# Kernel optimization log

Hardware: AMD Instinct MI355X
Metric: run time of the kernel (lower is better)

## Reference

```python
import jax, jax.numpy as jnp
import numpy as np

B, D, H, L = 2048, 4096, 1024, 64
LAM = 1.0  # topo_lambda


def setup_inputs() -> dict:
    key = jax.random.key(0)
    ks = jax.random.split(key, 5)
    def w(k, sh):
        fan_in = sh[0]
        return (jax.random.normal(k, sh, jnp.float32) * (1.0 / fan_in) ** 0.5)
    return {
        "x": jax.random.normal(ks[0], (B, D), jnp.float32),
        "W1": w(ks[1], (D, H)), "b1": jnp.zeros((H,), jnp.float32),
        "W2": w(ks[2], (H, L)), "b2": jnp.zeros((L,), jnp.float32),
        "W3": w(ks[3], (L, H)), "b3": jnp.zeros((H,), jnp.float32),
        "W4": w(ks[4], (H, D)), "b4": jnp.zeros((D,), jnp.float32),
        "latent_norm": jnp.ones((1,), jnp.float32),
    }


def _cdist(a):
    # pairwise euclidean distances [N, N], safe sqrt (zero grad on zero diag)
    sq = jnp.sum(a * a, axis=1)
    d2 = jnp.maximum(sq[:, None] + sq[None, :] - 2.0 * (a @ a.T), 0.0)
    pos = d2 > 0
    return jnp.where(pos, jnp.sqrt(jnp.where(pos, d2, 1.0)), 0.0)


def _mst_edges(d):
    # 0-dim persistence pairs == MST edges of the dense distance matrix.
    # Vectorized Prim's algorithm: scan of N-1 steps, O(N) work per step.
    n = d.shape[0]
    in_tree = jnp.zeros((n,), bool).at[0].set(True)
    min_dist = d[0]
    parent = jnp.zeros((n,), jnp.int32)

    def step(carry, _):
        in_tree, min_dist, parent = carry
        j = jnp.argmin(jnp.where(in_tree, jnp.inf, min_dist)).astype(jnp.int32)
        i = parent[j]
        in_tree = in_tree.at[j].set(True)
        better = (d[j] < min_dist) & ~in_tree
        min_dist = jnp.where(better, d[j], min_dist)
        parent = jnp.where(better, j, parent)
        return (in_tree, min_dist, parent), jnp.stack([i, j])

    _, edges = jax.lax.scan(step, (in_tree, min_dist, parent), None, length=n - 1)
    return edges  # [n-1, 2] int32


def _topo_signature(dx, dz):
    # pairing indices computed on detached distances (as in torch .detach())
    p1 = _mst_edges(jax.lax.stop_gradient(dx))
    p2 = _mst_edges(jax.lax.stop_gradient(dz))
    sig1 = dx[p1[:, 0], p1[:, 1]]
    sig1_2 = dz[p1[:, 0], p1[:, 1]]
    sig2 = dz[p2[:, 0], p2[:, 1]]
    sig2_1 = dx[p2[:, 0], p2[:, 1]]
    # match_edges == 'symmetric'
    return jnp.sum((sig1 - sig1_2) ** 2) + jnp.sum((sig2 - sig2_1) ** 2)


def reference(x, W1, b1, W2, b2, W3, b3, W4, b4, latent_norm):
    z = jax.nn.relu(x @ W1 + b1) @ W2 + b2            # [B, L]
    x_rec = jax.nn.relu(z @ W3 + b3) @ W4 + b4        # [B, D]
    rec_loss = jnp.mean((x_rec - x) ** 2)
    x_dist = _cdist(x)
    x_dist = x_dist / jnp.max(x_dist)
    z_dist = _cdist(z) / latent_norm[0]
    topo_loss = _topo_signature(x_dist, z_dist) / x.shape[0]
    loss = rec_loss + LAM * topo_loss
    return loss
```

## Files before the change

### kernel.cpp

```cpp
#include <hip/hip_runtime.h>
#include <hip/hip_bf16.h>

#define B_N 2048
#define D_N 4096
#define H_N 1024
#define L_N 64
#define NTILE 136
#define SPLK 4

typedef __attribute__((ext_vector_type(8))) short short8;
typedef __attribute__((ext_vector_type(4))) float float4_t;

#define ASG __attribute__((address_space(1)))
#define ASL __attribute__((address_space(3)))


__device__ inline float bf2f(unsigned short u) {
  union { unsigned u; float f; } v; v.u = ((unsigned)u) << 16; return v.f;
}
__device__ inline unsigned short f2bf(float f) {
  union { float f; unsigned u; } v; v.f = f;
  unsigned r = v.u + 0x7fffu + ((v.u >> 16) & 1u);
  return (unsigned short)(r >> 16);
}

__device__ inline float block_sum256(float v) {
  const int lane = threadIdx.x & 63, wave = threadIdx.x >> 6;
#pragma unroll
  for (int off = 32; off; off >>= 1) v += __shfl_xor(v, off);
  __shared__ float red_s[4];
  if (lane == 0) red_s[wave] = v;
  __syncthreads();
  return red_s[0] + red_s[1] + red_s[2] + red_s[3];
}

__device__ inline float block_max256(float v) {
  const int lane = threadIdx.x & 63, wave = threadIdx.x >> 6;
#pragma unroll
  for (int off = 32; off; off >>= 1) v = fmaxf(v, __shfl_xor(v, off));
  __shared__ float redm_s[4];
  if (lane == 0) redm_s[wave] = v;
  __syncthreads();
  return fmaxf(fmaxf(redm_s[0], redm_s[1]), fmaxf(redm_s[2], redm_s[3]));
}

__device__ inline void tri_idx(int b, int& tm, int& tn) {
  int m = (int)((sqrtf(8.f * (float)b + 1.f) - 1.f) * 0.5f);
  while ((m + 1) * (m + 2) / 2 <= b) ++m;
  while (m * (m + 1) / 2 > b) --m;
  tm = m;
  tn = b - m * (m + 1) / 2;
}


__global__ __launch_bounds__(256) void prep_x(const float* __restrict__ x,
                                              unsigned short* __restrict__ xb,
                                              float* __restrict__ sqx) {
  const int row = blockIdx.x;
  const int t = threadIdx.x;
  const float4* xr = (const float4*)(x + (size_t)row * D_N);
  float s = 0.f;
  for (int i = t; i < D_N / 4; i += 256) {
    float4 v = xr[i];
    s += v.x * v.x + v.y * v.y + v.z * v.z + v.w * v.w;
    ushort4 o;
    o.x = f2bf(v.x); o.y = f2bf(v.y); o.z = f2bf(v.z); o.w = f2bf(v.w);
    const int p = i >> 3;
    const int k31 = (4 * i) & 31;
    *(ushort4*)(xb + ((size_t)p * B_N + row) * 32 + k31) = o;
  }
  float tot = block_sum256(s);
  if (t == 0) sqx[row] = tot;
}

__global__ __launch_bounds__(256) void transpose_cast(const float* __restrict__ in,
                                                      unsigned short* __restrict__ out,
                                                      int R, int C) {
  __shared__ float tile[32][33];
  const int c0 = blockIdx.x * 32, r0 = blockIdx.y * 32;
  const int tx = threadIdx.x, ty = threadIdx.y;
#pragma unroll
  for (int i = 0; i < 32; i += 8)
    tile[ty + i][tx] = in[(size_t)(r0 + ty + i) * C + c0 + tx];
  __syncthreads();
#pragma unroll
  for (int i = 0; i < 32; i += 8)
    out[((size_t)(r0 >> 5) * C + c0 + ty + i) * 32 + tx] = f2bf(tile[tx][ty + i]);
}

__global__ __launch_bounds__(1024) void init_bor(float* __restrict__ accum,
                                                 int* __restrict__ comp,
                                                 int* __restrict__ cnt,
                                                 int* __restrict__ done) {
  const int t = threadIdx.x;
  if (t < 2) { accum[t] = 0.f; cnt[t] = 0; done[t] = 0; }
  for (int v = t; v < 2 * B_N; v += 1024) comp[v] = v & (B_N - 1);
}


__device__ inline void gemm_mainloop(const unsigned short* __restrict__ A,
                                     const unsigned short* __restrict__ Bt,
                                     int nrA, int nrB, int Klen, int m_base, int n_base,
                                     float4_t acc[4][4]) {
  __shared__ unsigned short lA[128 * 32];
  __shared__ unsigned short lB[128 * 32];
  const int t = threadIdx.x;
  const int wave = t >> 6;
  const int lane = t & 63;
  const int lrow = lane & 15;
  const int quad = lane >> 4;
  const int wm = (wave & 1) * 64;
  const int wn = (wave >> 1) * 64;

  const int srow = lane >> 2;
  const int scol = (lane & 3) * 8;

  for (int k0 = 0; k0 < Klen; k0 += 32) {
    const size_t pA = (size_t)(k0 >> 5) * nrA;
    const size_t pB = (size_t)(k0 >> 5) * nrB;
    __syncthreads();
#pragma unroll
    for (int q = 0; q < 2; ++q) {
      const int rbase = wave * 32 + q * 16;
      const int row = rbase + srow;
      __builtin_amdgcn_global_load_lds(
          (ASG void*)(A + (pA + m_base + row) * 32 + scol),
          (ASL void*)(lA + rbase * 32), 16, 0, 0);
      __builtin_amdgcn_global_load_lds(
          (ASG void*)(Bt + (pB + n_base + row) * 32 + scol),
          (ASL void*)(lB + rbase * 32), 16, 0, 0);
    }
    __syncthreads();
    short8 af[4], bfr[4];
#pragma unroll
    for (int f = 0; f < 4; ++f) {
      af[f]  = *(const short8*)(lA + (wm + f * 16 + lrow) * 32 + quad * 8);
      bfr[f] = *(const short8*)(lB + (wn + f * 16 + lrow) * 32 + quad * 8);
    }
#pragma unroll
    for (int fm = 0; fm < 4; ++fm)
#pragma unroll
      for (int fn = 0; fn < 4; ++fn)
        acc[fm][fn] = __builtin_amdgcn_mfma_f32_16x16x32_bf16(af[fm], bfr[fn],
                                                              acc[fm][fn], 0, 0, 0);
  }
}

__global__ __launch_bounds__(256) void gemm_splitk(const unsigned short* __restrict__ A,
                                                   const unsigned short* __restrict__ Bt,
                                                   int nrA, int nrB, int Kchunk, int N,
                                                   float* __restrict__ partial) {
  float4_t acc[4][4];
  float4_t z4 = {0.f, 0.f, 0.f, 0.f};
#pragma unroll
  for (int a = 0; a < 4; ++a)
#pragma unroll
    for (int b = 0; b < 4; ++b) acc[a][b] = z4;
  const int s = blockIdx.z;
  const int m_base = blockIdx.y * 128, n_base = blockIdx.x * 128;
  const size_t po = (size_t)(s * (Kchunk >> 5));
  gemm_mainloop(A + po * nrA * 32, Bt + po * nrB * 32, nrA, nrB, Kchunk,
                m_base, n_base, acc);
  const size_t MN = (size_t)gridDim.y * 128 * N;
  float* __restrict__ P = partial + (size_t)s * MN;
  const int t = threadIdx.x, wave = t >> 6, lane = t & 63;
  const int lrow = lane & 15, quad = lane >> 4;
  const int wm = (wave & 1) * 64, wn = (wave >> 1) * 64;
#pragma unroll
  for (int fm = 0; fm < 4; ++fm)
#pragma unroll
    for (int fn = 0; fn < 4; ++fn) {
      const int r0 = m_base + wm + fm * 16 + quad * 4;
      const int c = n_base + wn + fn * 16 + lrow;
#pragma unroll
      for (int r = 0; r < 4; ++r)
        P[(size_t)(r0 + r) * N + c] = acc[fm][fn][r];
    }
}

__global__ __launch_bounds__(256) void gemm_d2_tri(const unsigned short* __restrict__ xb,
                                                   float* __restrict__ partial) {
  float4_t acc[4][4];
  float4_t z4 = {0.f, 0.f, 0.f, 0.f};
#pragma unroll
  for (int a = 0; a < 4; ++a)
#pragma unroll
    for (int b = 0; b < 4; ++b) acc[a][b] = z4;
  const int s = blockIdx.z;
  int tm, tn;
  tri_idx(blockIdx.x, tm, tn);
  const size_t po = (size_t)(s * ((D_N / SPLK) >> 5)) * B_N * 32;
  gemm_mainloop(xb + po, xb + po, B_N, B_N, D_N / SPLK, tm * 128, tn * 128, acc);
  float* __restrict__ P = partial + ((size_t)s * NTILE + blockIdx.x) * 16384;
  const int t = threadIdx.x, wave = t >> 6, lane = t & 63;
  const int lrow = lane & 15, quad = lane >> 4;
  const int wm = (wave & 1) * 64, wn = (wave >> 1) * 64;
#pragma unroll
  for (int fm = 0; fm < 4; ++fm)
#pragma unroll
    for (int fn = 0; fn < 4; ++fn) {
      const int lr0 = wm + fm * 16 + quad * 4;
      const int lc = wn + fn * 16 + lrow;
#pragma unroll
      for (int r = 0; r < 4; ++r)
        P[(lr0 + r) * 128 + lc] = acc[fm][fn][r];
    }
}

__global__ __launch_bounds__(256) void fin_bias_relu(const float* __restrict__ partial,
                                                     const float* __restrict__ bias,
                                                     unsigned short* __restrict__ out) {
  const size_t MN = (size_t)B_N * H_N;
  const size_t i4 = ((size_t)blockIdx.x * 256 + threadIdx.x) * 4;
  float4 a = *(const float4*)(partial + i4);
#pragma unroll
  for (int s = 1; s < SPLK; ++s) {
    float4 p = *(const float4*)(partial + s * MN + i4);
    a.x += p.x; a.y += p.y; a.z += p.z; a.w += p.w;
  }
  const int row = (int)(i4 >> 10);
  const int k = (int)(i4 & (H_N - 1));
  float4 b = *(const float4*)(bias + k);
  ushort4 o;
  o.x = f2bf(fmaxf(a.x + b.x, 0.f));
  o.y = f2bf(fmaxf(a.y + b.y, 0.f));
  o.z = f2bf(fmaxf(a.z + b.z, 0.f));
  o.w = f2bf(fmaxf(a.w + b.w, 0.f));
  *(ushort4*)(out + ((size_t)(k >> 5) * B_N + row) * 32 + (k & 31)) = o;
}

__global__ __launch_bounds__(256) void fin_d2_tri(const float* __restrict__ partial,
                                                  const float* __restrict__ sq,
                                                  float* __restrict__ Out,
                                                  unsigned* __restrict__ max_slot) {
  const int tile = blockIdx.y;
  const int c0 = blockIdx.x * 32;
  int tm, tn;
  tri_idx(tile, tm, tn);
  __shared__ float lds[32][132];
  const int t = threadIdx.x;
  const int cc = (t & 7) * 4;
  float lmax = 0.f;
#pragma unroll
  for (int q = 0; q < 4; ++q) {
    const int r = (t >> 3) + 32 * q;
    const float* base = partial + (size_t)tile * 16384 + r * 128 + c0 + cc;
    float4 a = *(const float4*)base;
#pragma unroll
    for (int s = 1; s < SPLK; ++s) {
      float4 p = *(const float4*)(base + (size_t)s * NTILE * 16384);
      a.x += p.x; a.y += p.y; a.z += p.z; a.w += p.w;
    }
    const int i = tm * 128 + r;
    const float si = sq[i];
    float4 sj = *(const float4*)(sq + tn * 128 + c0 + cc);
    float4 v;
    v.x = fmaxf(si + sj.x - 2.f * a.x, 0.f);
    v.y = fmaxf(si + sj.y - 2.f * a.y, 0.f);
    v.z = fmaxf(si + sj.z - 2.f * a.z, 0.f);
    v.w = fmaxf(si + sj.w - 2.f * a.w, 0.f);
    *(float4*)(Out + (size_t)i * B_N + tn * 128 + c0 + cc) = v;
    lds[cc + 0][r] = v.x;
    lds[cc + 1][r] = v.y;
    lds[cc + 2][r] = v.z;
    lds[cc + 3][r] = v.w;
    lmax = fmaxf(lmax, fmaxf(fmaxf(v.x, v.y), fmaxf(v.z, v.w)));
  }
  __syncthreads();
#pragma unroll
  for (int m = 0; m < 4; ++m) {
    const int lin = t + 256 * m;
    const int cc2 = lin >> 5;
    const int r4 = (lin & 31) * 4;
    float4 w = *(const float4*)(&lds[cc2][r4]);
    *(float4*)(Out + (size_t)(tn * 128 + c0 + cc2) * B_N + tm * 128 + r4) = w;
  }
  float tot = block_max256(lmax);
  if (t == 0) atomicMax(max_slot, __float_as_uint(tot));
}

__global__ __launch_bounds__(256) void gemm_recloss(const unsigned short* __restrict__ A,
                                                    const unsigned short* __restrict__ Bt,
                                                    const float* __restrict__ bias,
                                                    const float* __restrict__ Xref,
                                                    float* __restrict__ acc_slot) {
  float4_t acc[4][4];
  float4_t z4 = {0.f, 0.f, 0.f, 0.f};
#pragma unroll
  for (int a = 0; a < 4; ++a)
#pragma unroll
    for (int b = 0; b < 4; ++b) acc[a][b] = z4;
  const int m_base = blockIdx.y * 128, n_base = blockIdx.x * 128;
  gemm_mainloop(A, Bt, B_N, D_N, H_N, m_base, n_base, acc);
  const int t = threadIdx.x, wave = t >> 6, lane = t & 63;
  const int lrow = lane & 15, quad = lane >> 4;
  const int wm = (wave & 1) * 64, wn = (wave >> 1) * 64;
  float local = 0.f;
#pragma unroll
  for (int fm = 0; fm < 4; ++fm)
#pragma unroll
    for (int fn = 0; fn < 4; ++fn) {
      const int r0 = m_base + wm + fm * 16 + quad * 4;
      const int c = n_base + wn + fn * 16 + lrow;
      const float bc = bias[c];
#pragma unroll
      for (int r = 0; r < 4; ++r) {
        float v = acc[fm][fn][r] + bc - Xref[(size_t)(r0 + r) * D_N + c];
        local += v * v;
      }
    }
  float tot = block_sum256(local);
  if (t == 0) atomicAdd(acc_slot, tot);
}


__global__ __launch_bounds__(256) void g2_k(const unsigned short* __restrict__ h1b,
                                            const float* __restrict__ W2,
                                            const float* __restrict__ b2,
                                            float* __restrict__ z,
                                            float* __restrict__ sqz) {
  const int col = threadIdx.x & 63;
  const int row = blockIdx.x * 4 + (threadIdx.x >> 6);
  float a0 = 0.f, a1 = 0.f, a2 = 0.f, a3 = 0.f;
  for (int p = 0; p < H_N / 32; ++p) {
    const unsigned short* hb = h1b + ((size_t)p * B_N + row) * 32;
    const float* wb = W2 + (p * 32) * L_N + col;
#pragma unroll
    for (int k2 = 0; k2 < 32; k2 += 4) {
      a0 += bf2f(hb[k2 + 0]) * wb[(k2 + 0) * L_N];
      a1 += bf2f(hb[k2 + 1]) * wb[(k2 + 1) * L_N];
      a2 += bf2f(hb[k2 + 2]) * wb[(k2 + 2) * L_N];
      a3 += bf2f(hb[k2 + 3]) * wb[(k2 + 3) * L_N];
    }
  }
  const float zv = (a0 + a1) + (a2 + a3) + b2[col];
  z[(size_t)row * L_N + col] = zv;
  float s = zv * zv;
#pragma unroll
  for (int off = 32; off; off >>= 1) s += __shfl_xor(s, off);
  if (col == 0) sqz[row] = s;
}

__global__ __launch_bounds__(256) void g3_k(const float* __restrict__ z,
                                            const float* __restrict__ W3,
                                            const float* __restrict__ b3,
                                            unsigned short* __restrict__ h2b) {
  const int t = threadIdx.x;
  const int col = blockIdx.y * 256 + t;
  const int r0 = blockIdx.x * 4;
  __shared__ float zr[4][64];
  zr[t >> 6][t & 63] = z[(size_t)(r0 + (t >> 6)) * L_N + (t & 63)];
  __syncthreads();
  const float bc = b3[col];
  float a0 = bc, a1 = bc, a2 = bc, a3 = bc;
#pragma unroll 8
  for (int k = 0; k < 64; ++k) {
    float w = W3[k * H_N + col];
    a0 += zr[0][k] * w;
    a1 += zr[1][k] * w;
    a2 += zr[2][k] * w;
    a3 += zr[3][k] * w;
  }
  const size_t base = ((size_t)(col >> 5) * B_N) * 32 + (col & 31);
  h2b[base + (size_t)(r0 + 0) * 32] = f2bf(fmaxf(a0, 0.f));
  h2b[base + (size_t)(r0 + 1) * 32] = f2bf(fmaxf(a1, 0.f));
  h2b[base + (size_t)(r0 + 2) * 32] = f2bf(fmaxf(a2, 0.f));
  h2b[base + (size_t)(r0 + 3) * 32] = f2bf(fmaxf(a3, 0.f));
}

__global__ __launch_bounds__(256) void d2z_k(const float* __restrict__ z,
                                             const float* __restrict__ sqz,
                                             float* __restrict__ d2z) {
  const int bi = blockIdx.y * 16, bj = blockIdx.x * 16;
  __shared__ float zi[16][65], zj[16][65];
  const int t = threadIdx.x;
  for (int idx = t; idx < 16 * 64; idx += 256) {
    const int r = idx >> 6, c = idx & 63;
    zi[r][c] = z[(size_t)(bi + r) * L_N + c];
    zj[r][c] = z[(size_t)(bj + r) * L_N + c];
  }
  __syncthreads();
  const int ti = t >> 4, tj = t & 15;
  float dot = 0.f;
#pragma unroll 8
  for (int k = 0; k < 64; ++k) dot += zi[ti][k] * zj[tj][k];
  float v = fmaxf(sqz[bi + ti] + sqz[bj + tj] - 2.f * dot, 0.f);
  d2z[(size_t)(bi + ti) * B_N + bj + tj] = v;
}

__global__ __launch_bounds__(256) void bor_scan(const float* __restrict__ d2x,
                                                const float* __restrict__ d2z,
                                                const int* __restrict__ comp,
                                                unsigned long long* __restrict__ rowbest,
                                                const int* __restrict__ done) {
  const int tree = blockIdx.y;
  if (done[tree]) return;
  const float* __restrict__ d2 = tree ? d2z : d2x;
  const int* __restrict__ cp = comp + tree * B_N;
  const int i = blockIdx.x;
  const int t = threadIdx.x;
  const int ci = cp[i];
  const float* __restrict__ row = d2 + (size_t)i * B_N;
  const unsigned ibase = (unsigned)(i << 11);
  unsigned long long k = ~0ull;
#pragma unroll
  for (int m = 0; m < 2; ++m) {
    const int j4 = (t + m * 256) * 4;
    float4 dv = *(const float4*)(row + j4);
    int4 cj = *(const int4*)(cp + j4);
    if (cj.x != ci) {
      unsigned long long key = (((unsigned long long)__float_as_uint(dv.x)) << 32) | (ibase | (unsigned)(j4 + 0));
      k = key < k ? key : k;
    }
    if (cj.y != ci) {
      unsigned long long key = (((unsigned long long)__float_as_uint(dv.y)) << 32) | (ibase | (unsigned)(j4 + 1));
      k = key < k ? key : k;
    }
    if (cj.z != ci) {
      unsigned long long key = (((unsigned long long)__float_as_uint(dv.z)) << 32) | (ibase | (unsigned)(j4 + 2));
      k = key < k ? key : k;
    }
    if (cj.w != ci) {
      unsigned long long key = (((unsigned long long)__float_as_uint(dv.w)) << 32) | (ibase | (unsigned)(j4 + 3));
      k = key < k ? key : k;
    }
  }
  const int lane = t & 63, wave = t >> 6;
#pragma unroll
  for (int off = 32; off; off >>= 1) {
    unsigned long long o = __shfl_xor(k, off);
    k = o < k ? o : k;
  }
  __shared__ unsigned long long wmin[4];
  if (lane == 0) wmin[wave] = k;
  __syncthreads();
  if (t == 0) {
    unsigned long long a = wmin[0] < wmin[1] ? wmin[0] : wmin[1];
    unsigned long long b = wmin[2] < wmin[3] ? wmin[2] : wmin[3];
    rowbest[tree * B_N + i] = (a < b) ? a : b;
  }
}

__global__ __launch_bounds__(1024) void bor_merge(const unsigned long long* __restrict__ rowbest,
                                                  int* __restrict__ comp,
                                                  int2* __restrict__ edges,
                                                  int* __restrict__ cnt,
                                                  int* __restrict__ done) {
  const int tree = blockIdx.x;
  if (done[tree]) return;
  const unsigned long long* __restrict__ rb = rowbest + tree * B_N;
  int* __restrict__ cp = comp + tree * B_N;
  int2* __restrict__ eo = edges + (size_t)tree * (B_N - 1);
  int* __restrict__ cn = cnt + tree;
  __shared__ unsigned long long bc[B_N];
  __shared__ int hk[B_N];
  __shared__ int allsame;
  const int t = threadIdx.x;

#pragma unroll
  for (int q = 0; q < 2; ++q) bc[t + q * 1024] = ~0ull;
  __syncthreads();

#pragma unroll
  for (int q = 0; q < 2; ++q) {
    const int i = t + q * 1024;
    const unsigned long long key = rb[i];
    if (key != ~0ull) atomicMin(&bc[cp[i]], key);
  }
  __syncthreads();

  unsigned long long mykey[2];
#pragma unroll
  for (int q = 0; q < 2; ++q) {
    const int c = t + q * 1024;
    const unsigned long long key = bc[c];
    mykey[q] = key;
    int h = c;
    if (key != ~0ull) h = cp[(unsigned)key & (unsigned)(B_N - 1)];
    hk[c] = h;
  }
  __syncthreads();

  int rloc[2];
#pragma unroll
  for (int q = 0; q < 2; ++q) {
    const int c = t + q * 1024;
    const unsigned long long key = mykey[q];
    const int h = hk[c];
    const int hh = hk[h];
    const bool valid = key != ~0ull;
    const bool two = (h != c) && (hh == c);
    rloc[q] = (two && c < h) ? c : h;
    if (valid && (!two || c < h)) {
      int e = atomicAdd(cn, 1);
      eo[e] = make_int2((int)((key >> 11) & (unsigned)(B_N - 1)),
                        (int)(key & (unsigned)(B_N - 1)));
    }
  }
  __syncthreads();
#pragma unroll
  for (int q = 0; q < 2; ++q) hk[t + q * 1024] = rloc[q];
  if (t == 0) allsame = 1;
  __syncthreads();

  for (int it = 0; it < 11; ++it) {
    const int v0 = hk[hk[t]];
    const int v1 = hk[hk[t + 1024]];
    __syncthreads();
    hk[t] = v0;
    hk[t + 1024] = v1;
    __syncthreads();
  }

#pragma unroll
  for (int q = 0; q < 2; ++q) {
    const int v = t + q * 1024;
    cp[v] = hk[cp[v]];
  }
  __syncthreads();
  const int c0v = cp[0];
  if (cp[t] != c0v || cp[t + 1024] != c0v) allsame = 0;
  __syncthreads();
  if (t == 0 && allsame) done[tree] = 1;
}

__global__ __launch_bounds__(256) void final_k(const float* __restrict__ d2x,
                                               const float* __restrict__ d2z,
                                               const int2* __restrict__ edges,
                                               const float* __restrict__ accum,
                                               const float* __restrict__ latent_norm,
                                               float* __restrict__ out) {
  const int t = threadIdx.x;
  const float maxd = sqrtf(__uint_as_float(((const unsigned*)accum)[1]));
  const float inv_maxd = 1.0f / maxd;
  const float inv_ln = 1.0f / latent_norm[0];
  float local = 0.f;
  for (int e = t; e < 2 * (B_N - 1); e += 256) {
    int2 ij = edges[e];
    size_t idx = (size_t)ij.x * B_N + ij.y;
    float xd = sqrtf(d2x[idx]) * inv_maxd;
    float zd = sqrtf(d2z[idx]) * inv_ln;
    float d = xd - zd;
    local += d * d;
  }
  float topo = block_sum256(local);
  if (t == 0)
    out[0] = accum[0] * (1.0f / ((float)B_N * (float)D_N)) + topo * (1.0f / (float)B_N);
}

extern "C" void kernel_launch(void* const* d_in, const int* in_sizes, int n_in,
                              void* d_out, int out_size, void* d_ws, size_t ws_size,
                              hipStream_t stream) {
  const float* x  = (const float*)d_in[0];
  const float* W1 = (const float*)d_in[1];
  const float* b1 = (const float*)d_in[2];
  const float* W2 = (const float*)d_in[3];
  const float* b2 = (const float*)d_in[4];
  const float* W3 = (const float*)d_in[5];
  const float* b3 = (const float*)d_in[6];
  const float* W4 = (const float*)d_in[7];
  const float* b4 = (const float*)d_in[8];
  const float* latent_norm = (const float*)d_in[9];
  float* out = (float*)d_out;

  char* ws = (char*)d_ws;
  size_t off = 0;
  auto alloc = [&](size_t bytes) {
    size_t o = off;
    off += (bytes + 255) & ~(size_t)255;
    return o;
  };
  unsigned short* xb   = (unsigned short*)(ws + alloc((size_t)B_N * D_N * 2));
  unsigned short* w1bt = (unsigned short*)(ws + alloc((size_t)H_N * D_N * 2));
  unsigned short* w4bt = (unsigned short*)(ws + alloc((size_t)D_N * H_N * 2));
  unsigned short* h1b  = (unsigned short*)(ws + alloc((size_t)B_N * H_N * 2));
  unsigned short* h2b  = (unsigned short*)(ws + alloc((size_t)B_N * H_N * 2));
  float* z    = (float*)(ws + alloc((size_t)B_N * L_N * 4));
  float* sqx  = (float*)(ws + alloc((size_t)B_N * 4));
  float* sqz  = (float*)(ws + alloc((size_t)B_N * 4));
  float* d2x  = (float*)(ws + alloc((size_t)B_N * B_N * 4));
  float* d2z  = (float*)(ws + alloc((size_t)B_N * B_N * 4));
  int2* edges = (int2*)(ws + alloc((size_t)2 * (B_N - 1) * sizeof(int2)));
  float* accum = (float*)(ws + alloc(256));
  int* comp   = (int*)(ws + alloc((size_t)2 * B_N * 4));
  unsigned long long* rowbest = (unsigned long long*)(ws + alloc((size_t)2 * B_N * 8));
  int* cnt    = (int*)(ws + alloc(256));
  int* done   = (int*)(ws + alloc(256));
  float* parts = (float*)(ws + alloc((size_t)SPLK * NTILE * 16384 * 4));

  init_bor<<<1, 1024, 0, stream>>>(accum, comp, cnt, done);
  prep_x<<<B_N, 256, 0, stream>>>(x, xb, sqx);
  transpose_cast<<<dim3(H_N / 32, D_N / 32), dim3(32, 8), 0, stream>>>(W1, w1bt, D_N, H_N);
  transpose_cast<<<dim3(D_N / 32, H_N / 32), dim3(32, 8), 0, stream>>>(W4, w4bt, H_N, D_N);

  gemm_splitk<<<dim3(H_N / 128, B_N / 128, SPLK), 256, 0, stream>>>(
      xb, w1bt, B_N, H_N, D_N / SPLK, H_N, parts);
  fin_bias_relu<<<(B_N * H_N) / 1024, 256, 0, stream>>>(parts, b1, h1b);

  g2_k<<<B_N / 4, 256, 0, stream>>>(h1b, W2, b2, z, sqz);
  g3_k<<<dim3(B_N / 4, H_N / 256), 256, 0, stream>>>(z, W3, b3, h2b);
  gemm_recloss<<<dim3(D_N / 128, B_N / 128), 256, 0, stream>>>(h2b, w4bt, b4, x, accum);

  gemm_d2_tri<<<dim3(NTILE, 1, SPLK), 256, 0, stream>>>(xb, parts);
  fin_d2_tri<<<dim3(4, NTILE), 256, 0, stream>>>(parts, sqx, d2x, (unsigned*)(accum + 1));

  d2z_k<<<dim3(B_N / 16, B_N / 16), 256, 0, stream>>>(z, sqz, d2z);

  for (int r = 0; r < 11; ++r) {
    bor_scan<<<dim3(B_N, 2), 256, 0, stream>>>(d2x, d2z, comp, rowbest, done);
    bor_merge<<<2, 1024, 0, stream>>>(rowbest, comp, edges, cnt, done);
  }
  final_k<<<1, 256, 0, stream>>>(d2x, d2z, edges, accum, latent_norm, out);
}
```

Measured before the change: 427.2 us.

## Precompute per-row nearest-neighbor lists to shortcut Boruvka row scans; merge setup kernels

Adds a top-16 nearest-neighbor kernel per row for both distance matrices. Each Boruvka scan round first checks these cached neighbors and skips the full 2048-wide row read when one lies in a different component. The init, prep and two transpose kernels are also merged into fewer launches. The cost is one extra full pass over both distance matrices plus 16 serial block reductions per row, paid back only if later rounds mostly take the fast path.

```diff
diff --git a/kernel.cpp b/kernel.cpp
--- a/kernel.cpp
+++ b/kernel.cpp
@@ -7,13 +7,13 @@
 #define L_N 64
 #define NTILE 136
 #define SPLK 4
+#define NNK 16
 
 typedef __attribute__((ext_vector_type(8))) short short8;
 typedef __attribute__((ext_vector_type(4))) float float4_t;
 
 #define ASG __attribute__((address_space(1)))
 #define ASL __attribute__((address_space(3)))
-
 
 __device__ inline float bf2f(unsigned short u) {
   union { unsigned u; float f; } v; v.u = ((unsigned)u) << 16; return v.f;
@@ -55,9 +55,18 @@
 
 __global__ __launch_bounds__(256) void prep_x(const float* __restrict__ x,
                                               unsigned short* __restrict__ xb,
-                                              float* __restrict__ sqx) {
+                                              float* __restrict__ sqx,
+                                              float* __restrict__ accum,
+                                              int* __restrict__ comp,
+                                              int* __restrict__ cnt,
+                                              int* __restrict__ done) {
   const int row = blockIdx.x;
   const int t = threadIdx.x;
+  if (row == B_N) {
+    if (t < 2) { accum[t] = 0.f; cnt[t] = 0; done[t] = 0; }
+    for (int v = t; v < 2 * B_N; v += 256) comp[v] = v & (B_N - 1);
+    return;
+  }
   const float4* xr = (const float4*)(x + (size_t)row * D_N);
   float s = 0.f;
   for (int i = t; i < D_N / 4; i += 256) {
@@ -73,11 +82,18 @@
   if (t == 0) sqx[row] = tot;
 }
 
-__global__ __launch_bounds__(256) void transpose_cast(const float* __restrict__ in,
-                                                      unsigned short* __restrict__ out,
-                                                      int R, int C) {
+__global__ __launch_bounds__(256) void transpose2(const float* __restrict__ W1,
+                                                  const float* __restrict__ W4,
+                                                  unsigned short* __restrict__ w1bt,
+                                                  unsigned short* __restrict__ w4bt) {
   __shared__ float tile[32][33];
-  const int c0 = blockIdx.x * 32, r0 = blockIdx.y * 32;
+  int b = blockIdx.x;
+  const float* in;
+  unsigned short* out;
+  int C, bx, by;
+  if (b < 4096) { in = W1; out = w1bt; C = H_N; bx = b & 31;  by = b >> 5; }
+  else { b -= 4096; in = W4; out = w4bt; C = D_N; bx = b & 127; by = b >> 7; }
+  const int c0 = bx * 32, r0 = by * 32;
   const int tx = threadIdx.x, ty = threadIdx.y;
 #pragma unroll
   for (int i = 0; i < 32; i += 8)
@@ -86,15 +102,6 @@
 #pragma unroll
   for (int i = 0; i < 32; i += 8)
     out[((size_t)(r0 >> 5) * C + c0 + ty + i) * 32 + tx] = f2bf(tile[tx][ty + i]);
-}
-
-__global__ __launch_bounds__(1024) void init_bor(float* __restrict__ accum,
-                                                 int* __restrict__ comp,
-                                                 int* __restrict__ cnt,
-                                                 int* __restrict__ done) {
-  const int t = threadIdx.x;
-  if (t < 2) { accum[t] = 0.f; cnt[t] = 0; done[t] = 0; }
-  for (int v = t; v < 2 * B_N; v += 1024) comp[v] = v & (B_N - 1);
 }
 
 
@@ -388,9 +395,55 @@
   d2z[(size_t)(bi + ti) * B_N + bj + tj] = v;
 }
 
+__global__ __launch_bounds__(256) void topk_k(const float* __restrict__ d2x,
+                                              const float* __restrict__ d2z,
+                                              unsigned long long* __restrict__ nn) {
+  const int tree = blockIdx.y;
+  const float* __restrict__ d2 = tree ? d2z : d2x;
+  const int i = blockIdx.x;
+  const int t = threadIdx.x;
+  const float* __restrict__ row = d2 + (size_t)i * B_N;
+  const unsigned ibase = (unsigned)(i << 11);
+  float4 v0 = *(const float4*)(row + t * 8);
+  float4 v1 = *(const float4*)(row + t * 8 + 4);
+  unsigned long long key[8];
+  const float vv[8] = {v0.x, v0.y, v0.z, v0.w, v1.x, v1.y, v1.z, v1.w};
+#pragma unroll
+  for (int q = 0; q < 8; ++q) {
+    const int j = t * 8 + q;
+    key[q] = (j == i) ? ~0ull
+                      : ((((unsigned long long)__float_as_uint(vv[q])) << 32) |
+                         (ibase | (unsigned)j));
+  }
+  unsigned long long* __restrict__ out = nn + ((size_t)tree * B_N + i) * NNK;
+  __shared__ unsigned long long wmin_s[4];
+  const int lane = t & 63, wave = t >> 6;
+  for (int p = 0; p < NNK; ++p) {
+    unsigned long long k = key[0];
+#pragma unroll
+    for (int q = 1; q < 8; ++q) k = key[q] < k ? key[q] : k;
+#pragma unroll
+    for (int off = 32; off; off >>= 1) {
+      unsigned long long o = __shfl_xor(k, off);
+      k = o < k ? o : k;
+    }
+    if (lane == 0) wmin_s[wave] = k;
+    __syncthreads();
+    unsigned long long a = wmin_s[0] < wmin_s[1] ? wmin_s[0] : wmin_s[1];
+    unsigned long long b = wmin_s[2] < wmin_s[3] ? wmin_s[2] : wmin_s[3];
+    const unsigned long long w = a < b ? a : b;
+    if (t == 0) out[p] = w;
+#pragma unroll
+    for (int q = 0; q < 8; ++q)
+      if (key[q] == w) key[q] = ~0ull;
+    __syncthreads();
+  }
+}
+
 __global__ __launch_bounds__(256) void bor_scan(const float* __restrict__ d2x,
                                                 const float* __restrict__ d2z,
                                                 const int* __restrict__ comp,
+                                                const unsigned long long* __restrict__ nn,
                                                 unsigned long long* __restrict__ rowbest,
                                                 const int* __restrict__ done) {
   const int tree = blockIdx.y;
@@ -400,6 +453,27 @@
   const int i = blockIdx.x;
   const int t = threadIdx.x;
   const int ci = cp[i];
+  __shared__ unsigned long long fastkey;
+  __shared__ int needfull;
+  if (t < 64) {
+    unsigned long long k = ~0ull;
+    bool cross = false;
+    if (t < NNK) {
+      k = nn[((size_t)tree * B_N + i) * NNK + t];
+      cross = cp[(unsigned)k & (unsigned)(B_N - 1)] != ci;
+    }
+    const unsigned long long m = __ballot(cross);
+    if (t == 0) needfull = (m == 0ull);
+    if (m) {
+      const int wl = __builtin_ctzll(m);
+      if (t == wl) fastkey = k;
+    }
+  }
+  __syncthreads();
+  if (!needfull) {
+    if (t == 0) rowbest[tree * B_N + i] = fastkey;
+    return;
+  }
   const float* __restrict__ row = d2 + (size_t)i * B_N;
   const unsigned ibase = (unsigned)(i << 11);
   unsigned long long k = ~0ull;
@@ -584,14 +658,13 @@
   float* accum = (float*)(ws + alloc(256));
   int* comp   = (int*)(ws + alloc((size_t)2 * B_N * 4));
   unsigned long long* rowbest = (unsigned long long*)(ws + alloc((size_t)2 * B_N * 8));
+  unsigned long long* nn = (unsigned long long*)(ws + alloc((size_t)2 * B_N * NNK * 8));
   int* cnt    = (int*)(ws + alloc(256));
   int* done   = (int*)(ws + alloc(256));
   float* parts = (float*)(ws + alloc((size_t)SPLK * NTILE * 16384 * 4));
 
-  init_bor<<<1, 1024, 0, stream>>>(accum, comp, cnt, done);
-  prep_x<<<B_N, 256, 0, stream>>>(x, xb, sqx);
-  transpose_cast<<<dim3(H_N / 32, D_N / 32), dim3(32, 8), 0, stream>>>(W1, w1bt, D_N, H_N);
-  transpose_cast<<<dim3(D_N / 32, H_N / 32), dim3(32, 8), 0, stream>>>(W4, w4bt, H_N, D_N);
+  prep_x<<<B_N + 1, 256, 0, stream>>>(x, xb, sqx, accum, comp, cnt, done);
+  transpose2<<<8192, dim3(32, 8), 0, stream>>>(W1, W4, w1bt, w4bt);
 
   gemm_splitk<<<dim3(H_N / 128, B_N / 128, SPLK), 256, 0, stream>>>(
       xb, w1bt, B_N, H_N, D_N / SPLK, H_N, parts);
@@ -606,8 +679,9 @@
 
   d2z_k<<<dim3(B_N / 16, B_N / 16), 256, 0, stream>>>(z, sqz, d2z);
 
+  topk_k<<<dim3(B_N, 2), 256, 0, stream>>>(d2x, d2z, nn);
   for (int r = 0; r < 11; ++r) {
-    bor_scan<<<dim3(B_N, 2), 256, 0, stream>>>(d2x, d2z, comp, rowbest, done);
+    bor_scan<<<dim3(B_N, 2), 256, 0, stream>>>(d2x, d2z, comp, nn, rowbest, done);
     bor_merge<<<2, 1024, 0, stream>>>(rowbest, comp, edges, cnt, done);
   }
   final_k<<<1, 256, 0, stream>>>(d2x, d2z, edges, accum, latent_norm, out);
```

Result: slower. 462.0 us (+8.1%).

## Merge independent kernels into combined launches and skip unchanged Boruvka row scans

Applied to the files above, without the earlier changes.

Independent kernels are merged into shared launches that dispatch on block index: the prep/cast/init kernels, the two split-K GEMMs, the two finalize kernels, g3 with d2z, and the recon-loss GEMM with the first Boruvka scan. This cuts launch count and lets independent work fill the GPU together. The G1 and D2 GEMMs now use separate partial buffers so they can run in the same launch. bor_scan also skips a row when its previous best edge still points to another component, since that row's minimum cannot have changed. This skip depends on rowbest staying valid across rounds, and merging a GEMM with the row scan can leave some blocks imbalanced.

```diff
diff --git a/kernel.cpp b/kernel.cpp
--- a/kernel.cpp
+++ b/kernel.cpp
@@ -14,7 +14,6 @@
 #define ASG __attribute__((address_space(1)))
 #define ASL __attribute__((address_space(3)))
 
-
 __device__ inline float bf2f(unsigned short u) {
   union { unsigned u; float f; } v; v.u = ((unsigned)u) << 16; return v.f;
 }
@@ -52,33 +51,53 @@
   tn = b - m * (m + 1) / 2;
 }
 
-
-__global__ __launch_bounds__(256) void prep_x(const float* __restrict__ x,
-                                              unsigned short* __restrict__ xb,
-                                              float* __restrict__ sqx) {
-  const int row = blockIdx.x;
-  const int t = threadIdx.x;
-  const float4* xr = (const float4*)(x + (size_t)row * D_N);
-  float s = 0.f;
-  for (int i = t; i < D_N / 4; i += 256) {
-    float4 v = xr[i];
-    s += v.x * v.x + v.y * v.y + v.z * v.z + v.w * v.w;
-    ushort4 o;
-    o.x = f2bf(v.x); o.y = f2bf(v.y); o.z = f2bf(v.z); o.w = f2bf(v.w);
-    const int p = i >> 3;
-    const int k31 = (4 * i) & 31;
-    *(ushort4*)(xb + ((size_t)p * B_N + row) * 32 + k31) = o;
-  }
-  float tot = block_sum256(s);
-  if (t == 0) sqx[row] = tot;
-}
-
-__global__ __launch_bounds__(256) void transpose_cast(const float* __restrict__ in,
-                                                      unsigned short* __restrict__ out,
-                                                      int R, int C) {
+__global__ __launch_bounds__(256) void mega_prep(const float* __restrict__ x,
+                                                 const float* __restrict__ W1,
+                                                 const float* __restrict__ W4,
+                                                 unsigned short* __restrict__ xb,
+                                                 unsigned short* __restrict__ w1bt,
+                                                 unsigned short* __restrict__ w4bt,
+                                                 float* __restrict__ sqx,
+                                                 float* __restrict__ accum,
+                                                 int* __restrict__ comp,
+                                                 unsigned long long* __restrict__ rowbest,
+                                                 int* __restrict__ cnt,
+                                                 int* __restrict__ done) {
+  const int b = blockIdx.x;
+  const int t = threadIdx.x;
+  if (b < B_N) {
+    const float4* xr = (const float4*)(x + (size_t)b * D_N);
+    float s = 0.f;
+    for (int i = t; i < D_N / 4; i += 256) {
+      float4 v = xr[i];
+      s += v.x * v.x + v.y * v.y + v.z * v.z + v.w * v.w;
+      ushort4 o;
+      o.x = f2bf(v.x); o.y = f2bf(v.y); o.z = f2bf(v.z); o.w = f2bf(v.w);
+      const int p = i >> 3;
+      const int k31 = (4 * i) & 31;
+      *(ushort4*)(xb + ((size_t)p * B_N + b) * 32 + k31) = o;
+    }
+    float tot = block_sum256(s);
+    if (t == 0) sqx[b] = tot;
+    return;
+  }
+  if (b == B_N) {
+    if (t < 2) { accum[t] = 0.f; cnt[t] = 0; done[t] = 0; }
+    for (int v = t; v < 2 * B_N; v += 256) {
+      comp[v] = v & (B_N - 1);
+      rowbest[v] = ~0ull;
+    }
+    return;
+  }
+  int tb = b - (B_N + 1);
+  const float* in;
+  unsigned short* out;
+  int C, bx, by;
+  if (tb < 4096) { in = W1; out = w1bt; C = H_N; bx = tb & 31;  by = tb >> 5; }
+  else { tb -= 4096; in = W4; out = w4bt; C = D_N; bx = tb & 127; by = tb >> 7; }
+  const int c0 = bx * 32, r0 = by * 32;
+  const int tx = t & 31, ty = t >> 5;
   __shared__ float tile[32][33];
-  const int c0 = blockIdx.x * 32, r0 = blockIdx.y * 32;
-  const int tx = threadIdx.x, ty = threadIdx.y;
 #pragma unroll
   for (int i = 0; i < 32; i += 8)
     tile[ty + i][tx] = in[(size_t)(r0 + ty + i) * C + c0 + tx];
@@ -87,16 +106,6 @@
   for (int i = 0; i < 32; i += 8)
     out[((size_t)(r0 >> 5) * C + c0 + ty + i) * 32 + tx] = f2bf(tile[tx][ty + i]);
 }
-
-__global__ __launch_bounds__(1024) void init_bor(float* __restrict__ accum,
-                                                 int* __restrict__ comp,
-                                                 int* __restrict__ cnt,
-                                                 int* __restrict__ done) {
-  const int t = threadIdx.x;
-  if (t < 2) { accum[t] = 0.f; cnt[t] = 0; done[t] = 0; }
-  for (int v = t; v < 2 * B_N; v += 1024) comp[v] = v & (B_N - 1);
-}
-
 
 __device__ inline void gemm_mainloop(const unsigned short* __restrict__ A,
                                      const unsigned short* __restrict__ Bt,
@@ -111,7 +120,6 @@
   const int quad = lane >> 4;
   const int wm = (wave & 1) * 64;
   const int wn = (wave >> 1) * 64;
-
   const int srow = lane >> 2;
   const int scol = (lane & 3) * 8;
 
@@ -146,105 +154,103 @@
   }
 }
 
-__global__ __launch_bounds__(256) void gemm_splitk(const unsigned short* __restrict__ A,
-                                                   const unsigned short* __restrict__ Bt,
-                                                   int nrA, int nrB, int Kchunk, int N,
-                                                   float* __restrict__ partial) {
+__global__ __launch_bounds__(256) void mega_gemm(const unsigned short* __restrict__ xb,
+                                                 const unsigned short* __restrict__ w1bt,
+                                                 float* __restrict__ partsG1,
+                                                 float* __restrict__ partsD2) {
   float4_t acc[4][4];
   float4_t z4 = {0.f, 0.f, 0.f, 0.f};
 #pragma unroll
   for (int a = 0; a < 4; ++a)
 #pragma unroll
-    for (int b = 0; b < 4; ++b) acc[a][b] = z4;
-  const int s = blockIdx.z;
-  const int m_base = blockIdx.y * 128, n_base = blockIdx.x * 128;
-  const size_t po = (size_t)(s * (Kchunk >> 5));
-  gemm_mainloop(A + po * nrA * 32, Bt + po * nrB * 32, nrA, nrB, Kchunk,
-                m_base, n_base, acc);
-  const size_t MN = (size_t)gridDim.y * 128 * N;
-  float* __restrict__ P = partial + (size_t)s * MN;
+    for (int b2 = 0; b2 < 4; ++b2) acc[a][b2] = z4;
+  const int b = blockIdx.x;
   const int t = threadIdx.x, wave = t >> 6, lane = t & 63;
   const int lrow = lane & 15, quad = lane >> 4;
   const int wm = (wave & 1) * 64, wn = (wave >> 1) * 64;
-#pragma unroll
-  for (int fm = 0; fm < 4; ++fm)
-#pragma unroll
-    for (int fn = 0; fn < 4; ++fn) {
-      const int r0 = m_base + wm + fm * 16 + quad * 4;
-      const int c = n_base + wn + fn * 16 + lrow;
-#pragma unroll
-      for (int r = 0; r < 4; ++r)
-        P[(size_t)(r0 + r) * N + c] = acc[fm][fn][r];
-    }
-}
-
-__global__ __launch_bounds__(256) void gemm_d2_tri(const unsigned short* __restrict__ xb,
-                                                   float* __restrict__ partial) {
-  float4_t acc[4][4];
-  float4_t z4 = {0.f, 0.f, 0.f, 0.f};
-#pragma unroll
-  for (int a = 0; a < 4; ++a)
-#pragma unroll
-    for (int b = 0; b < 4; ++b) acc[a][b] = z4;
-  const int s = blockIdx.z;
-  int tm, tn;
-  tri_idx(blockIdx.x, tm, tn);
-  const size_t po = (size_t)(s * ((D_N / SPLK) >> 5)) * B_N * 32;
-  gemm_mainloop(xb + po, xb + po, B_N, B_N, D_N / SPLK, tm * 128, tn * 128, acc);
-  float* __restrict__ P = partial + ((size_t)s * NTILE + blockIdx.x) * 16384;
-  const int t = threadIdx.x, wave = t >> 6, lane = t & 63;
-  const int lrow = lane & 15, quad = lane >> 4;
-  const int wm = (wave & 1) * 64, wn = (wave >> 1) * 64;
-#pragma unroll
-  for (int fm = 0; fm < 4; ++fm)
-#pragma unroll
-    for (int fn = 0; fn < 4; ++fn) {
-      const int lr0 = wm + fm * 16 + quad * 4;
-      const int lc = wn + fn * 16 + lrow;
-#pragma unroll
-      for (int r = 0; r < 4; ++r)
-        P[(lr0 + r) * 128 + lc] = acc[fm][fn][r];
-    }
-}
-
-__global__ __launch_bounds__(256) void fin_bias_relu(const float* __restrict__ partial,
-                                                     const float* __restrict__ bias,
-                                                     unsigned short* __restrict__ out) {
-  const size_t MN = (size_t)B_N * H_N;
-  const size_t i4 = ((size_t)blockIdx.x * 256 + threadIdx.x) * 4;
-  float4 a = *(const float4*)(partial + i4);
-#pragma unroll
-  for (int s = 1; s < SPLK; ++s) {
-    float4 p = *(const float4*)(partial + s * MN + i4);
-    a.x += p.x; a.y += p.y; a.z += p.z; a.w += p.w;
-  }
-  const int row = (int)(i4 >> 10);
-  const int k = (int)(i4 & (H_N - 1));
-  float4 b = *(const float4*)(bias + k);
-  ushort4 o;
-  o.x = f2bf(fmaxf(a.x + b.x, 0.f));
-  o.y = f2bf(fmaxf(a.y + b.y, 0.f));
-  o.z = f2bf(fmaxf(a.z + b.z, 0.f));
-  o.w = f2bf(fmaxf(a.w + b.w, 0.f));
-  *(ushort4*)(out + ((size_t)(k >> 5) * B_N + row) * 32 + (k & 31)) = o;
-}
-
-__global__ __launch_bounds__(256) void fin_d2_tri(const float* __restrict__ partial,
-                                                  const float* __restrict__ sq,
-                                                  float* __restrict__ Out,
-                                                  unsigned* __restrict__ max_slot) {
-  const int tile = blockIdx.y;
-  const int c0 = blockIdx.x * 32;
+
+  if (b < 512) {
+    const int s = b >> 7;
+    const int tt = b & 127;
+    const int m_base = (tt >> 3) * 128, n_base = (tt & 7) * 128;
+    const size_t po = (size_t)(s * 32);
+    gemm_mainloop(xb + po * B_N * 32, w1bt + po * H_N * 32, B_N, H_N, D_N / SPLK,
+                  m_base, n_base, acc);
+    float* __restrict__ P = partsG1 + (size_t)s * B_N * H_N;
+#pragma unroll
+    for (int fm = 0; fm < 4; ++fm)
+#pragma unroll
+      for (int fn = 0; fn < 4; ++fn) {
+        const int r0 = m_base + wm + fm * 16 + quad * 4;
+        const int c = n_base + wn + fn * 16 + lrow;
+#pragma unroll
+        for (int r = 0; r < 4; ++r)
+          P[(size_t)(r0 + r) * H_N + c] = acc[fm][fn][r];
+      }
+  } else {
+    const int c = b - 512;
+    const int s = c / NTILE;
+    const int tt = c - s * NTILE;
+    const int tile = (tt & 7) * 17 + (tt >> 3);
+    int tm, tn;
+    tri_idx(tile, tm, tn);
+    const size_t po = (size_t)(s * 32) * B_N * 32;
+    gemm_mainloop(xb + po, xb + po, B_N, B_N, D_N / SPLK, tm * 128, tn * 128, acc);
+    float* __restrict__ P = partsD2 + ((size_t)s * NTILE + tile) * 16384;
+#pragma unroll
+    for (int fm = 0; fm < 4; ++fm)
+#pragma unroll
+      for (int fn = 0; fn < 4; ++fn) {
+        const int lr0 = wm + fm * 16 + quad * 4;
+        const int lc = wn + fn * 16 + lrow;
+#pragma unroll
+        for (int r = 0; r < 4; ++r)
+          P[(lr0 + r) * 128 + lc] = acc[fm][fn][r];
+      }
+  }
+}
+
+__global__ __launch_bounds__(256) void mega_fin(const float* __restrict__ partsG1,
+                                                const float* __restrict__ partsD2,
+                                                const float* __restrict__ bias,
+                                                const float* __restrict__ sq,
+                                                unsigned short* __restrict__ h1b,
+                                                float* __restrict__ d2x,
+                                                unsigned* __restrict__ max_slot) {
+  const int b = blockIdx.x;
+  const int t = threadIdx.x;
+  if (b < 2048) {
+    const size_t MN = (size_t)B_N * H_N;
+    const size_t i4 = ((size_t)b * 256 + t) * 4;
+    float4 a = *(const float4*)(partsG1 + i4);
+#pragma unroll
+    for (int s = 1; s < SPLK; ++s) {
+      float4 p = *(const float4*)(partsG1 + s * MN + i4);
+      a.x += p.x; a.y += p.y; a.z += p.z; a.w += p.w;
+    }
+    const int row = (int)(i4 >> 10);
+    const int k = (int)(i4 & (H_N - 1));
+    float4 bb = *(const float4*)(bias + k);
+    ushort4 o;
+    o.x = f2bf(fmaxf(a.x + bb.x, 0.f));
+    o.y = f2bf(fmaxf(a.y + bb.y, 0.f));
+    o.z = f2bf(fmaxf(a.z + bb.z, 0.f));
+    o.w = f2bf(fmaxf(a.w + bb.w, 0.f));
+    *(ushort4*)(h1b + ((size_t)(k >> 5) * B_N + row) * 32 + (k & 31)) = o;
+    return;
+  }
+  const int cidx = b - 2048;
+  const int tile = cidx >> 2;
+  const int c0 = (cidx & 3) * 32;
   int tm, tn;
   tri_idx(tile, tm, tn);
   __shared__ float lds[32][132];
-  const int t = threadIdx.x;
   const int cc = (t & 7) * 4;
   float lmax = 0.f;
 #pragma unroll
   for (int q = 0; q < 4; ++q) {
     const int r = (t >> 3) + 32 * q;
-    const float* base = partial + (size_t)tile * 16384 + r * 128 + c0 + cc;
+    const float* base = partsD2 + (size_t)tile * 16384 + r * 128 + c0 + cc;
     float4 a = *(const float4*)base;
 #pragma unroll
     for (int s = 1; s < SPLK; ++s) {
@@ -259,7 +265,7 @@
     v.y = fmaxf(si + sj.y - 2.f * a.y, 0.f);
     v.z = fmaxf(si + sj.z - 2.f * a.z, 0.f);
     v.w = fmaxf(si + sj.w - 2.f * a.w, 0.f);
-    *(float4*)(Out + (size_t)i * B_N + tn * 128 + c0 + cc) = v;
+    *(float4*)(d2x + (size_t)i * B_N + tn * 128 + c0 + cc) = v;
     lds[cc + 0][r] = v.x;
     lds[cc + 1][r] = v.y;
     lds[cc + 2][r] = v.z;
@@ -273,46 +279,11 @@
     const int cc2 = lin >> 5;
     const int r4 = (lin & 31) * 4;
     float4 w = *(const float4*)(&lds[cc2][r4]);
-    *(float4*)(Out + (size_t)(tn * 128 + c0 + cc2) * B_N + tm * 128 + r4) = w;
+    *(float4*)(d2x + (size_t)(tn * 128 + c0 + cc2) * B_N + tm * 128 + r4) = w;
   }
   float tot = block_max256(lmax);
   if (t == 0) atomicMax(max_slot, __float_as_uint(tot));
 }
-
-__global__ __launch_bounds__(256) void gemm_recloss(const unsigned short* __restrict__ A,
-                                                    const unsigned short* __restrict__ Bt,
-                                                    const float* __restrict__ bias,
-                                                    const float* __restrict__ Xref,
-                                                    float* __restrict__ acc_slot) {
-  float4_t acc[4][4];
-  float4_t z4 = {0.f, 0.f, 0.f, 0.f};
-#pragma unroll
-  for (int a = 0; a < 4; ++a)
-#pragma unroll
-    for (int b = 0; b < 4; ++b) acc[a][b] = z4;
-  const int m_base = blockIdx.y * 128, n_base = blockIdx.x * 128;
-  gemm_mainloop(A, Bt, B_N, D_N, H_N, m_base, n_base, acc);
-  const int t = threadIdx.x, wave = t >> 6, lane = t & 63;
-  const int lrow = lane & 15, quad = lane >> 4;
-  const int wm = (wave & 1) * 64, wn = (wave >> 1) * 64;
-  float local = 0.f;
-#pragma unroll
-  for (int fm = 0; fm < 4; ++fm)
-#pragma unroll
-    for (int fn = 0; fn < 4; ++fn) {
-      const int r0 = m_base + wm + fm * 16 + quad * 4;
-      const int c = n_base + wn + fn * 16 + lrow;
-      const float bc = bias[c];
-#pragma unroll
-      for (int r = 0; r < 4; ++r) {
-        float v = acc[fm][fn][r] + bc - Xref[(size_t)(r0 + r) * D_N + c];
-        local += v * v;
-      }
-    }
-  float tot = block_sum256(local);
-  if (t == 0) atomicAdd(acc_slot, tot);
-}
-
 
 __global__ __launch_bounds__(256) void g2_k(const unsigned short* __restrict__ h1b,
                                             const float* __restrict__ W2,
@@ -341,43 +312,45 @@
   if (col == 0) sqz[row] = s;
 }
 
-__global__ __launch_bounds__(256) void g3_k(const float* __restrict__ z,
-                                            const float* __restrict__ W3,
-                                            const float* __restrict__ b3,
-                                            unsigned short* __restrict__ h2b) {
-  const int t = threadIdx.x;
-  const int col = blockIdx.y * 256 + t;
-  const int r0 = blockIdx.x * 4;
-  __shared__ float zr[4][64];
-  zr[t >> 6][t & 63] = z[(size_t)(r0 + (t >> 6)) * L_N + (t & 63)];
-  __syncthreads();
-  const float bc = b3[col];
-  float a0 = bc, a1 = bc, a2 = bc, a3 = bc;
+__global__ __launch_bounds__(256) void mega_g3_d2z(const float* __restrict__ z,
+                                                   const float* __restrict__ W3,
+                                                   const float* __restrict__ b3,
+                                                   const float* __restrict__ sqz,
+                                                   unsigned short* __restrict__ h2b,
+                                                   float* __restrict__ d2z) {
+  const int b = blockIdx.x;
+  const int t = threadIdx.x;
+  if (b < 2048) {
+    const int rg = b & 511, cg = b >> 9;
+    const int col = cg * 256 + t;
+    const int r0 = rg * 4;
+    __shared__ float zr[4][64];
+    zr[t >> 6][t & 63] = z[(size_t)(r0 + (t >> 6)) * L_N + (t & 63)];
+    __syncthreads();
+    const float bc = b3[col];
+    float a0 = bc, a1 = bc, a2 = bc, a3 = bc;
 #pragma unroll 8
-  for (int k = 0; k < 64; ++k) {
-    float w = W3[k * H_N + col];
-    a0 += zr[0][k] * w;
-    a1 += zr[1][k] * w;
-    a2 += zr[2][k] * w;
-    a3 += zr[3][k] * w;
-  }
-  const size_t base = ((size_t)(col >> 5) * B_N) * 32 + (col & 31);
-  h2b[base + (size_t)(r0 + 0) * 32] = f2bf(fmaxf(a0, 0.f));
-  h2b[base + (size_t)(r0 + 1) * 32] = f2bf(fmaxf(a1, 0.f));
-  h2b[base + (size_t)(r0 + 2) * 32] = f2bf(fmaxf(a2, 0.f));
-  h2b[base + (size_t)(r0 + 3) * 32] = f2bf(fmaxf(a3, 0.f));
-}
-
-__global__ __launch_bounds__(256) void d2z_k(const float* __restrict__ z,
-                                             const float* __restrict__ sqz,
-                                             float* __restrict__ d2z) {
-  const int bi = blockIdx.y * 16, bj = blockIdx.x * 16;
+    for (int k = 0; k < 64; ++k) {
+      float w = W3[k * H_N + col];
+      a0 += zr[0][k] * w;
+      a1 += zr[1][k] * w;
+      a2 += zr[2][k] * w;
+      a3 += zr[3][k] * w;
+    }
+    const size_t base = ((size_t)(col >> 5) * B_N) * 32 + (col & 31);
+    h2b[base + (size_t)(r0 + 0) * 32] = f2bf(fmaxf(a0, 0.f));
+    h2b[base + (size_t)(r0 + 1) * 32] = f2bf(fmaxf(a1, 0.f));
+    h2b[base + (size_t)(r0 + 2) * 32] = f2bf(fmaxf(a2, 0.f));
+    h2b[base + (size_t)(r0 + 3) * 32] = f2bf(fmaxf(a3, 0.f));
+    return;
+  }
+  const int c = b - 2048;
+  const int bi = (c >> 7) * 16, bj = (c & 127) * 16;
   __shared__ float zi[16][65], zj[16][65];
-  const int t = threadIdx.x;
   for (int idx = t; idx < 16 * 64; idx += 256) {
-    const int r = idx >> 6, c = idx & 63;
-    zi[r][c] = z[(size_t)(bi + r) * L_N + c];
-    zj[r][c] = z[(size_t)(bj + r) * L_N + c];
+    const int r = idx >> 6, cc = idx & 63;
+    zi[r][cc] = z[(size_t)(bi + r) * L_N + cc];
+    zj[r][cc] = z[(size_t)(bj + r) * L_N + cc];
   }
   __syncthreads();
   const int ti = t >> 4, tj = t & 15;
@@ -386,6 +359,95 @@
   for (int k = 0; k < 64; ++k) dot += zi[ti][k] * zj[tj][k];
   float v = fmaxf(sqz[bi + ti] + sqz[bj + tj] - 2.f * dot, 0.f);
   d2z[(size_t)(bi + ti) * B_N + bj + tj] = v;
+}
+
+__device__ inline void scan_row(const float* __restrict__ row, const int* __restrict__ cp,
+                                int i, int ci, unsigned long long* __restrict__ dst) {
+  const int t = threadIdx.x;
+  const unsigned ibase = (unsigned)(i << 11);
+  unsigned long long k = ~0ull;
+#pragma unroll
+  for (int m = 0; m < 2; ++m) {
+    const int j4 = (t + m * 256) * 4;
+    float4 dv = *(const float4*)(row + j4);
+    int4 cj = *(const int4*)(cp + j4);
+    if (cj.x != ci) {
+      unsigned long long key = (((unsigned long long)__float_as_uint(dv.x)) << 32) | (ibase | (unsigned)(j4 + 0));
+      k = key < k ? key : k;
+    }
+    if (cj.y != ci) {
+      unsigned long long key = (((unsigned long long)__float_as_uint(dv.y)) << 32) | (ibase | (unsigned)(j4 + 1));
+      k = key < k ? key : k;
+    }
+    if (cj.z != ci) {
+      unsigned long long key = (((unsigned long long)__float_as_uint(dv.z)) << 32) | (ibase | (unsigned)(j4 + 2));
+      k = key < k ? key : k;
+    }
+    if (cj.w != ci) {
+      unsigned long long key = (((unsigned long long)__float_as_uint(dv.w)) << 32) | (ibase | (unsigned)(j4 + 3));
+      k = key < k ? key : k;
+    }
+  }
+  const int lane = t & 63, wave = t >> 6;
+#pragma unroll
+  for (int off = 32; off; off >>= 1) {
+    unsigned long long o = __shfl_xor(k, off);
+    k = o < k ? o : k;
+  }
+  __shared__ unsigned long long wmin[4];
+  if (lane == 0) wmin[wave] = k;
+  __syncthreads();
+  if (t == 0) {
+    unsigned long long a = wmin[0] < wmin[1] ? wmin[0] : wmin[1];
+    unsigned long long b = wmin[2] < wmin[3] ? wmin[2] : wmin[3];
+    *dst = (a < b) ? a : b;
+  }
+}
+
+__global__ __launch_bounds__(256) void mega_recloss_scan0(
+    const unsigned short* __restrict__ h2b, const unsigned short* __restrict__ w4bt,
+    const float* __restrict__ bias, const float* __restrict__ Xref,
+    float* __restrict__ acc_slot,
+    const float* __restrict__ d2x, const float* __restrict__ d2z,
+    const int* __restrict__ comp, unsigned long long* __restrict__ rowbest) {
+  const int b = blockIdx.x;
+  const int t = threadIdx.x;
+  if (b < 512) {
+    float4_t acc[4][4];
+    float4_t z4 = {0.f, 0.f, 0.f, 0.f};
+#pragma unroll
+    for (int a = 0; a < 4; ++a)
+#pragma unroll
+      for (int b2 = 0; b2 < 4; ++b2) acc[a][b2] = z4;
+    const int m_base = (b >> 5) * 128, n_base = (b & 31) * 128;
+    gemm_mainloop(h2b, w4bt, B_N, D_N, H_N, m_base, n_base, acc);
+    const int wave = t >> 6, lane = t & 63;
+    const int lrow = lane & 15, quad = lane >> 4;
+    const int wm = (wave & 1) * 64, wn = (wave >> 1) * 64;
+    float local = 0.f;
+#pragma unroll
+    for (int fm = 0; fm < 4; ++fm)
+#pragma unroll
+      for (int fn = 0; fn < 4; ++fn) {
+        const int r0 = m_base + wm + fm * 16 + quad * 4;
+        const int c = n_base + wn + fn * 16 + lrow;
+        const float bc = bias[c];
+#pragma unroll
+        for (int r = 0; r < 4; ++r) {
+          float v = acc[fm][fn][r] + bc - Xref[(size_t)(r0 + r) * D_N + c];
+          local += v * v;
+        }
+      }
+    float tot = block_sum256(local);
+    if (t == 0) atomicAdd(acc_slot, tot);
+    return;
+  }
+  const int c = b - 512;
+  const int i = c & (B_N - 1);
+  const int tree = c >> 11;
+  const float* __restrict__ d2 = tree ? d2z : d2x;
+  const int* __restrict__ cp = comp + tree * B_N;
+  scan_row(d2 + (size_t)i * B_N, cp, i, cp[i], rowbest + tree * B_N + i);
 }
 
 __global__ __launch_bounds__(256) void bor_scan(const float* __restrict__ d2x,
@@ -395,50 +457,16 @@
                                                 const int* __restrict__ done) {
   const int tree = blockIdx.y;
   if (done[tree]) return;
+  const int i = blockIdx.x;
+  const int* __restrict__ cp = comp + tree * B_N;
+  const int ci = cp[i];
+  const unsigned long long prev = rowbest[tree * B_N + i];
+  if (prev != ~0ull) {
+    const int j = (int)(prev & (unsigned)(B_N - 1));
+    if (cp[j] != ci) return;
+  }
   const float* __restrict__ d2 = tree ? d2z : d2x;
-  const int* __restrict__ cp = comp + tree * B_N;
-  const int i = blockIdx.x;
-  const int t = threadIdx.x;
-  const int ci = cp[i];
-  const float* __restrict__ row = d2 + (size_t)i * B_N;
-  const unsigned ibase = (unsigned)(i << 11);
-  unsigned long long k = ~0ull;
-#pragma unroll
-  for (int m = 0; m < 2; ++m) {
-    const int j4 = (t + m * 256) * 4;
-    float4 dv = *(const float4*)(row + j4);
-    int4 cj = *(const int4*)(cp + j4);
-    if (cj.x != ci) {
-      unsigned long long key = (((unsigned long long)__float_as_uint(dv.x)) << 32) | (ibase | (unsigned)(j4 + 0));
-      k = key < k ? key : k;
-    }
-    if (cj.y != ci) {
-      unsigned long long key = (((unsigned long long)__float_as_uint(dv.y)) << 32) | (ibase | (unsigned)(j4 + 1));
-      k = key < k ? key : k;
-    }
-    if (cj.z != ci) {
-      unsigned long long key = (((unsigned long long)__float_as_uint(dv.z)) << 32) | (ibase | (unsigned)(j4 + 2));
-      k = key < k ? key : k;
-    }
-    if (cj.w != ci) {
-      unsigned long long key = (((unsigned long long)__float_as_uint(dv.w)) << 32) | (ibase | (unsigned)(j4 + 3));
-      k = key < k ? key : k;
-    }
-  }
-  const int lane = t & 63, wave = t >> 6;
-#pragma unroll
-  for (int off = 32; off; off >>= 1) {
-    unsigned long long o = __shfl_xor(k, off);
-    k = o < k ? o : k;
-  }
-  __shared__ unsigned long long wmin[4];
-  if (lane == 0) wmin[wave] = k;
-  __syncthreads();
-  if (t == 0) {
-    unsigned long long a = wmin[0] < wmin[1] ? wmin[0] : wmin[1];
-    unsigned long long b = wmin[2] < wmin[3] ? wmin[2] : wmin[3];
-    rowbest[tree * B_N + i] = (a < b) ? a : b;
-  }
+  scan_row(d2 + (size_t)i * B_N, cp, i, ci, rowbest + tree * B_N + i);
 }
 
 __global__ __launch_bounds__(1024) void bor_merge(const unsigned long long* __restrict__ rowbest,
@@ -460,7 +488,6 @@
 #pragma unroll
   for (int q = 0; q < 2; ++q) bc[t + q * 1024] = ~0ull;
   __syncthreads();
-
 #pragma unroll
   for (int q = 0; q < 2; ++q) {
     const int i = t + q * 1024;
@@ -586,27 +613,20 @@
   unsigned long long* rowbest = (unsigned long long*)(ws + alloc((size_t)2 * B_N * 8));
   int* cnt    = (int*)(ws + alloc(256));
   int* done   = (int*)(ws + alloc(256));
-  float* parts = (float*)(ws + alloc((size_t)SPLK * NTILE * 16384 * 4));
-
-  init_bor<<<1, 1024, 0, stream>>>(accum, comp, cnt, done);
-  prep_x<<<B_N, 256, 0, stream>>>(x, xb, sqx);
-  transpose_cast<<<dim3(H_N / 32, D_N / 32), dim3(32, 8), 0, stream>>>(W1, w1bt, D_N, H_N);
-  transpose_cast<<<dim3(D_N / 32, H_N / 32), dim3(32, 8), 0, stream>>>(W4, w4bt, H_N, D_N);
-
-  gemm_splitk<<<dim3(H_N / 128, B_N / 128, SPLK), 256, 0, stream>>>(
-      xb, w1bt, B_N, H_N, D_N / SPLK, H_N, parts);
-  fin_bias_relu<<<(B_N * H_N) / 1024, 256, 0, stream>>>(parts, b1, h1b);
-
+  float* partsG1 = (float*)(ws + alloc((size_t)SPLK * B_N * H_N * 4));
+  float* partsD2 = (float*)(ws + alloc((size_t)SPLK * NTILE * 16384 * 4));
+
+  mega_prep<<<B_N + 1 + 8192, 256, 0, stream>>>(x, W1, W4, xb, w1bt, w4bt, sqx,
+                                                accum, comp, rowbest, cnt, done);
+  mega_gemm<<<512 + SPLK * NTILE, 256, 0, stream>>>(xb, w1bt, partsG1, partsD2);
+  mega_fin<<<2048 + 4 * NTILE, 256, 0, stream>>>(partsG1, partsD2, b1, sqx, h1b, d2x,
+                                                 (unsigned*)(accum + 1));
   g2_k<<<B_N / 4, 256, 0, stream>>>(h1b, W2, b2, z, sqz);
-  g3_k<<<dim3(B_N / 4, H_N / 256), 256, 0, stream>>>(z, W3, b3, h2b);
-  gemm_recloss<<<dim3(D_N / 128, B_N / 128), 256, 0, stream>>>(h2b, w4bt, b4, x, accum);
-
-  gemm_d2_tri<<<dim3(NTILE, 1, SPLK), 256, 0, stream>>>(xb, parts);
-  fin_d2_tri<<<dim3(4, NTILE), 256, 0, stream>>>(parts, sqx, d2x, (unsigned*)(accum + 1));
-
-  d2z_k<<<dim3(B_N / 16, B_N / 16), 256, 0, stream>>>(z, sqz, d2z);
-
-  for (int r = 0; r < 11; ++r) {
+  mega_g3_d2z<<<2048 + 16384, 256, 0, stream>>>(z, W3, b3, sqz, h2b, d2z);
+  mega_recloss_scan0<<<512 + 2 * B_N, 256, 0, stream>>>(h2b, w4bt, b4, x, accum,
+                                                        d2x, d2z, comp, rowbest);
+  bor_merge<<<2, 1024, 0, stream>>>(rowbest, comp, edges, cnt, done);
+  for (int r = 1; r < 11; ++r) {
     bor_scan<<<dim3(B_N, 2), 256, 0, stream>>>(d2x, d2z, comp, rowbest, done);
     bor_merge<<<2, 1024, 0, stream>>>(rowbest, comp, edges, cnt, done);
   }
```

New measurement: 407.0 us, median of 3. 1.05x faster.
